# Optimization experiments

Measured on AMD Instinct MI355X. Metric: run time of the kernel, lower is better.

The kernel has to match this reference:

```python
import jax, jax.numpy as jnp
import numpy as np

D, K, H1, H2 = 768, 4, 512, 256
B = 16384

def layer_norm(x, g, b, eps=1e-5):
    mu = jnp.mean(x, axis=-1, keepdims=True)
    xc = x - mu
    var = jnp.mean(xc * xc, axis=-1, keepdims=True)
    return xc * jax.lax.rsqrt(var + eps) * g + b

def setup_inputs() -> dict:
    key = jax.random.key(0)
    ks = jax.random.split(key, 8)
    def lin(k, fan_in, fan_out):
        bound = 1.0 / np.sqrt(fan_in)
        kw, kb = jax.random.split(k)
        W = jax.random.uniform(kw, (fan_in, fan_out), jnp.float32, -bound, bound)
        b = jax.random.uniform(kb, (fan_out,), jnp.float32, -bound, bound)
        return W, b
    W1, b1 = lin(ks[0], D, H1)
    W2, b2 = lin(ks[1], H1, H2)
    Wd, bd = lin(ks[2], H2, K * D)
    Wa, ba = lin(ks[3], H2, D)
    return {
        "embeddings": jax.random.normal(ks[4], (B, D), jnp.float32),
        "W1": W1, "b1": b1, "g1": jnp.ones((H1,), jnp.float32), "be1": jnp.zeros((H1,), jnp.float32),
        "W2": W2, "b2": b2, "g2": jnp.ones((H2,), jnp.float32), "be2": jnp.zeros((H2,), jnp.float32),
        "Wd": Wd, "bd": bd, "Wa": Wa, "ba": ba,
    }

def _forward(embeddings, W1, b1, g1, be1, W2, b2, g2, be2, Wd, bd, Wa, ba):
    h = jax.nn.relu(layer_norm(embeddings @ W1 + b1, g1, be1))  # (B, H1)
    h = jax.nn.relu(layer_norm(h @ W2 + b2, g2, be2))           # (B, H2)
    W_flat = h @ Wd + bd                                         # (B, K*D)
    W = W_flat.reshape(-1, K, D)
    attn = jax.nn.softmax(h @ Wa + ba, axis=-1)                  # (B, D)
    W = W * attn[:, None, :]
    # sequential Gram-Schmidt over k (small fixed K, unrolled)
    ortho = []
    for i in range(K):
        v = W[:, i, :]
        for u in ortho:
            proj = jnp.sum(v * u, axis=-1, keepdims=True)
            v = v - proj * u
        norm = jnp.maximum(jnp.linalg.norm(v, axis=-1, keepdims=True), 1e-12)
        ortho.append(v / norm)
    W_ortho = jnp.stack(ortho, axis=1)  # (B, K, D)
    return W_ortho, attn

def reference(embeddings, W1, b1, g1, be1, W2, b2, g2, be2, Wd, bd, Wa, ba):
    return _forward(embeddings, W1, b1, g1, be1, W2, b2, g2, be2, Wd, bd, Wa, ba)
```

## Files before the change

kernel.cpp:

```cpp
#include <hip/hip_runtime.h>
#include <hip/hip_bf16.h>

#define BSZ 16384
#define DD  768
#define KK  4
#define NH1 512
#define NH2 256
#define ND  (KK * DD)

typedef __bf16 bf16x8 __attribute__((ext_vector_type(8)));
typedef float  f32x4  __attribute__((ext_vector_type(4)));

static __device__ __forceinline__ float bf2f(ushort u) {
    union { unsigned int i; float f; } v; v.i = (unsigned int)u << 16; return v.f;
}
static __device__ __forceinline__ ushort f2bf(float f) {
    return __bfloat16_as_ushort(__float2bfloat16(f));
}
static __device__ __forceinline__ void gload_lds16(const void* g, void* l) {
    __builtin_amdgcn_global_load_lds(
        (const __attribute__((address_space(1))) void*)g,
        (__attribute__((address_space(3))) void*)l, 16, 0, 0);
}

__global__ __launch_bounds__(256) void k_prep(
    const float* __restrict__ emb, ushort* __restrict__ embb,
    const float* __restrict__ W1, ushort* __restrict__ W1t,
    const float* __restrict__ W2, ushort* __restrict__ W2t,
    const float* __restrict__ Wd, ushort* __restrict__ Wdt,
    const float* __restrict__ Wa, ushort* __restrict__ Wat)
{
    __shared__ float tile[32][33];
    const int bid = blockIdx.x;
    const int t = threadIdx.x;

    if (bid < 2048) {
        const int n8 = BSZ * DD / 8;
        const int stride = 2048 * 256;
        for (int i = bid * 256 + t; i < n8; i += stride) {
            float4 a = *(const float4*)&emb[(size_t)i * 8];
            float4 b = *(const float4*)&emb[(size_t)i * 8 + 4];
            ushort u[8];
            u[0] = f2bf(a.x); u[1] = f2bf(a.y); u[2] = f2bf(a.z); u[3] = f2bf(a.w);
            u[4] = f2bf(b.x); u[5] = f2bf(b.y); u[6] = f2bf(b.z); u[7] = f2bf(b.w);
            *(int4*)&embb[(size_t)i * 8] = *(int4*)u;
        }
        return;
    }

    const float* src; ushort* dst; int R, C, rb0, cb0;
    if (bid < 2432)      { int l = bid - 2048; src = W1; dst = W1t; R = DD;  C = NH1;
                           cb0 = (l & 15) * 32; rb0 = (l >> 4) * 32; }
    else if (bid < 2560) { int l = bid - 2432; src = W2; dst = W2t; R = NH1; C = NH2;
                           cb0 = (l & 7) * 32;  rb0 = (l >> 3) * 32; }
    else if (bid < 3328) { int l = bid - 2560; src = Wd; dst = Wdt; R = NH2; C = ND;
                           cb0 = (l % 96) * 32; rb0 = (l / 96) * 32; }
    else                 { int l = bid - 3328; src = Wa; dst = Wat; R = NH2; C = DD;
                           cb0 = (l % 24) * 32; rb0 = (l / 24) * 32; }

    const int r = t >> 5, c = t & 31;
    #pragma unroll
    for (int i = 0; i < 4; ++i)
        tile[r + i * 8][c] = src[(size_t)(rb0 + r + i * 8) * C + cb0 + c];
    __syncthreads();
    #pragma unroll
    for (int i = 0; i < 4; ++i)
        dst[(size_t)(cb0 + r + i * 8) * R + rb0 + c] = f2bf(tile[c][r + i * 8]);
}

__global__ __launch_bounds__(256) void k1_gemm(
    const ushort* __restrict__ embb, const ushort* __restrict__ W1t,
    const float* __restrict__ b1, ushort* __restrict__ h1raw)
{
    __shared__ ushort smem[2 * 128 * 64];
    ushort* Asm = smem;
    ushort* Bsm = smem + 128 * 64;

    const int t    = threadIdx.x;
    const int lane = t & 63;
    const int wid  = t >> 6;
    const int wm   = wid >> 1;
    const int wn   = wid & 1;
    const int l16  = lane & 15;
    const int sl0  = lane >> 4;
    const int g4   = (lane >> 4) * 4;

    const int srow = lane >> 3;
    const int ssl  = (lane & 7) ^ srow;

    const int rb = blockIdx.y * 128;
    const int cb = blockIdx.x * 128;

    f32x4 acc[4][4] = {};

    for (int ks = 0; ks < 12; ++ks) {
        const int k0 = ks * 64;
        __syncthreads();
        #pragma unroll
        for (int i = 0; i < 4; ++i) {
            const int stripe = wid * 4 + i;
            const int row    = stripe * 8 + srow;
            gload_lds16(&embb[(size_t)(rb + row) * DD + k0 + ssl * 8],
                        &Asm[stripe * 512]);
            gload_lds16(&W1t [(size_t)(cb + row) * DD + k0 + ssl * 8],
                        &Bsm[stripe * 512]);
        }
        __syncthreads();

        #pragma unroll
        for (int kk = 0; kk < 2; ++kk) {
            const int slot = kk * 4 + sl0;
            bf16x8 af[4], bfr[4];
            #pragma unroll
            for (int m = 0; m < 4; ++m) {
                const int R = wm * 64 + m * 16 + l16;
                af[m] = *(const bf16x8*)&Asm[R * 64 + (slot ^ (R & 7)) * 8];
            }
            #pragma unroll
            for (int n = 0; n < 4; ++n) {
                const int R = wn * 64 + n * 16 + l16;
                bfr[n] = *(const bf16x8*)&Bsm[R * 64 + (slot ^ (R & 7)) * 8];
            }
            #pragma unroll
            for (int m = 0; m < 4; ++m)
                #pragma unroll
                for (int n = 0; n < 4; ++n)
                    acc[m][n] = __builtin_amdgcn_mfma_f32_16x16x32_bf16(
                        af[m], bfr[n], acc[m][n], 0, 0, 0);
        }
    }

    float bv[4];
    #pragma unroll
    for (int n = 0; n < 4; ++n)
        bv[n] = b1[cb + wn * 64 + n * 16 + l16];

    __syncthreads();
    #pragma unroll
    for (int m = 0; m < 4; ++m)
        #pragma unroll
        for (int n = 0; n < 4; ++n)
            #pragma unroll
            for (int j = 0; j < 4; ++j)
                smem[(wm * 64 + m * 16 + g4 + j) * 128 + wn * 64 + n * 16 + l16] =
                    f2bf(acc[m][n][j] + bv[n]);
    __syncthreads();
    #pragma unroll
    for (int i = 0; i < 8; ++i) {
        int ch  = t + i * 256;
        int row = ch >> 4;
        int q   = ch & 15;
        *(int4*)&h1raw[(size_t)(rb + row) * NH1 + cb + q * 8] =
            *(const int4*)&smem[row * 128 + q * 8];
    }
}

__global__ __launch_bounds__(512) void k2_mfma(
    const ushort* __restrict__ h1raw, const ushort* __restrict__ W2t,
    const float* __restrict__ g1, const float* __restrict__ be1,
    const float* __restrict__ b2, const float* __restrict__ g2,
    const float* __restrict__ be2, ushort* __restrict__ h2)
{
    __shared__ ushort Ah[8 * 2048];
    __shared__ ushort Bsm[256 * 64];
    __shared__ float red[8][32][2];
    __shared__ float stats[32][2];

    const int t    = threadIdx.x;
    const int lane = t & 63;
    const int wid  = t >> 6;
    const int l16  = lane & 15;
    const int sl0  = lane >> 4;
    const int g4   = (lane >> 4) * 4;
    const int rb   = blockIdx.x * 32;

    const int srow = lane >> 3;
    const int ssl  = (lane & 7) ^ srow;

    #pragma unroll
    for (int i = 0; i < 4; ++i) {
        const int s  = wid * 4 + i;
        const int ks = s >> 2;
        const int st = s & 3;
        const int row = st * 8 + srow;
        gload_lds16(&h1raw[(size_t)(rb + row) * NH1 + ks * 64 + ssl * 8],
                    &Ah[ks * 2048 + st * 512]);
    }
    __syncthreads();

    {
        const int r  = t >> 4;
        const int j  = t & 15;
        const int ks = j >> 1;
        const int hf = j & 1;
        ushort u[4][8];
        float s = 0.f, q2 = 0.f;
        #pragma unroll
        for (int qi = 0; qi < 4; ++qi) {
            const int q = hf * 4 + qi;
            *(int4*)u[qi] = *(const int4*)
                &Ah[ks * 2048 + (r >> 3) * 512 + (r & 7) * 64 + ((q ^ (r & 7)) * 8)];
            #pragma unroll
            for (int e = 0; e < 8; ++e) {
                float x = bf2f(u[qi][e]);
                s += x; q2 += x * x;
            }
        }
        #pragma unroll
        for (int off = 8; off; off >>= 1) {
            s  += __shfl_xor(s, off);
            q2 += __shfl_xor(q2, off);
        }
        const float mu  = s * (1.f / NH1);
        const float var = q2 * (1.f / NH1) - mu * mu;
        const float rs  = rsqrtf(var + 1e-5f);
        #pragma unroll
        for (int qi = 0; qi < 4; ++qi) {
            const int q = hf * 4 + qi;
            const int col = ks * 64 + q * 8;
            float gv[8], ev[8];
            *(float4*)&gv[0] = *(const float4*)&g1[col];
            *(float4*)&gv[4] = *(const float4*)&g1[col + 4];
            *(float4*)&ev[0] = *(const float4*)&be1[col];
            *(float4*)&ev[4] = *(const float4*)&be1[col + 4];
            #pragma unroll
            for (int e = 0; e < 8; ++e) {
                float x = bf2f(u[qi][e]);
                u[qi][e] = f2bf(fmaxf(fmaf((x - mu) * rs, gv[e], ev[e]), 0.f));
            }
            *(int4*)&Ah[ks * 2048 + (r >> 3) * 512 + (r & 7) * 64 + ((q ^ (r & 7)) * 8)]
                = *(int4*)u[qi];
        }
    }

    f32x4 acc[2][2] = {};

    for (int ks = 0; ks < 8; ++ks) {
        const int k0 = ks * 64;
        __syncthreads();
        #pragma unroll
        for (int i = 0; i < 4; ++i) {
            const int s   = wid * 4 + i;
            const int row = s * 8 + srow;
            gload_lds16(&W2t[(size_t)row * NH1 + k0 + ssl * 8],
                        &Bsm[s * 512]);
        }
        __syncthreads();

        #pragma unroll
        for (int kk = 0; kk < 2; ++kk) {
            const int slot = kk * 4 + sl0;
            bf16x8 af[2], bfr[2];
            #pragma unroll
            for (int m = 0; m < 2; ++m) {
                const int R = m * 16 + l16;
                af[m] = *(const bf16x8*)
                    &Ah[ks * 2048 + R * 64 + (slot ^ (R & 7)) * 8];
            }
            #pragma unroll
            for (int n = 0; n < 2; ++n) {
                const int R = wid * 32 + n * 16 + l16;
                bfr[n] = *(const bf16x8*)&Bsm[R * 64 + (slot ^ (R & 7)) * 8];
            }
            #pragma unroll
            for (int m = 0; m < 2; ++m)
                #pragma unroll
                for (int n = 0; n < 2; ++n)
                    acc[m][n] = __builtin_amdgcn_mfma_f32_16x16x32_bf16(
                        af[m], bfr[n], acc[m][n], 0, 0, 0);
        }
    }

    float bv[2];
    #pragma unroll
    for (int n = 0; n < 2; ++n) bv[n] = b2[wid * 32 + n * 16 + l16];
    #pragma unroll
    for (int m = 0; m < 2; ++m)
        #pragma unroll
        for (int n = 0; n < 2; ++n)
            #pragma unroll
            for (int j = 0; j < 4; ++j) acc[m][n][j] += bv[n];

    #pragma unroll
    for (int m = 0; m < 2; ++m)
        #pragma unroll
        for (int j = 0; j < 4; ++j) {
            float p = 0.f, q = 0.f;
            #pragma unroll
            for (int n = 0; n < 2; ++n) {
                float v = acc[m][n][j];
                p += v; q += v * v;
            }
            #pragma unroll
            for (int off = 8; off; off >>= 1) {
                p += __shfl_xor(p, off);
                q += __shfl_xor(q, off);
            }
            if (l16 == 0) {
                red[wid][m * 16 + g4 + j][0] = p;
                red[wid][m * 16 + g4 + j][1] = q;
            }
        }
    __syncthreads();
    if (t < 32) {
        float S = 0.f, S2 = 0.f;
        #pragma unroll
        for (int w = 0; w < 8; ++w) { S += red[w][t][0]; S2 += red[w][t][1]; }
        float mu  = S  * (1.f / NH2);
        float var = S2 * (1.f / NH2) - mu * mu;
        stats[t][0] = mu;
        stats[t][1] = rsqrtf(var + 1e-5f);
    }
    __syncthreads();

    float gv[2], ev[2];
    #pragma unroll
    for (int n = 0; n < 2; ++n) {
        int col = wid * 32 + n * 16 + l16;
        gv[n] = g2[col]; ev[n] = be2[col];
    }
    ushort* dst = h2 + (size_t)rb * NH2;
    #pragma unroll
    for (int m = 0; m < 2; ++m)
        #pragma unroll
        for (int j = 0; j < 4; ++j) {
            int row = m * 16 + g4 + j;
            float mu = stats[row][0], rs = stats[row][1];
            #pragma unroll
            for (int n = 0; n < 2; ++n) {
                float val = fmaxf(fmaf((acc[m][n][j] - mu) * rs, gv[n], ev[n]), 0.f);
                dst[(size_t)row * NH2 + wid * 32 + n * 16 + l16] = f2bf(val);
            }
        }
}

__global__ __launch_bounds__(256) void k_gemm_wd_mfma(
    const ushort* __restrict__ h2, const ushort* __restrict__ Wdt,
    const float* __restrict__ bd, ushort* __restrict__ outw)
{
    __shared__ ushort smem[2 * 128 * 64];
    ushort* Asm = smem;
    ushort* Bsm = smem + 128 * 64;

    const int t    = threadIdx.x;
    const int lane = t & 63;
    const int wid  = t >> 6;
    const int wm   = wid >> 1;
    const int wn   = wid & 1;
    const int l16  = lane & 15;
    const int sl0  = lane >> 4;
    const int g4   = (lane >> 4) * 4;

    const int srow = lane >> 3;
    const int ssl  = (lane & 7) ^ srow;

    const int rb = blockIdx.y * 128;
    const int cb = blockIdx.x * 128;

    f32x4 acc[4][4] = {};

    for (int ks = 0; ks < 4; ++ks) {
        const int k0 = ks * 64;
        __syncthreads();
        #pragma unroll
        for (int i = 0; i < 4; ++i) {
            const int stripe = wid * 4 + i;
            const int row    = stripe * 8 + srow;
            gload_lds16(&h2 [(size_t)(rb + row) * NH2 + k0 + ssl * 8],
                        &Asm[stripe * 512]);
            gload_lds16(&Wdt[(size_t)(cb + row) * NH2 + k0 + ssl * 8],
                        &Bsm[stripe * 512]);
        }
        __syncthreads();

        #pragma unroll
        for (int kk = 0; kk < 2; ++kk) {
            const int slot = kk * 4 + sl0;
            bf16x8 af[4], bfr[4];
            #pragma unroll
            for (int m = 0; m < 4; ++m) {
                const int R = wm * 64 + m * 16 + l16;
                af[m] = *(const bf16x8*)&Asm[R * 64 + (slot ^ (R & 7)) * 8];
            }
            #pragma unroll
            for (int n = 0; n < 4; ++n) {
                const int R = wn * 64 + n * 16 + l16;
                bfr[n] = *(const bf16x8*)&Bsm[R * 64 + (slot ^ (R & 7)) * 8];
            }
            #pragma unroll
            for (int m = 0; m < 4; ++m)
                #pragma unroll
                for (int n = 0; n < 4; ++n)
                    acc[m][n] = __builtin_amdgcn_mfma_f32_16x16x32_bf16(
                        af[m], bfr[n], acc[m][n], 0, 0, 0);
        }
    }

    float bv[4];
    #pragma unroll
    for (int n = 0; n < 4; ++n)
        bv[n] = bd[cb + wn * 64 + n * 16 + l16];

    __syncthreads();
    #pragma unroll
    for (int m = 0; m < 4; ++m)
        #pragma unroll
        for (int n = 0; n < 4; ++n)
            #pragma unroll
            for (int j = 0; j < 4; ++j)
                smem[(wm * 64 + m * 16 + g4 + j) * 128 + wn * 64 + n * 16 + l16] =
                    f2bf(acc[m][n][j] + bv[n]);
    __syncthreads();
    #pragma unroll
    for (int i = 0; i < 8; ++i) {
        int ch  = t + i * 256;
        int row = ch >> 4;
        int q   = ch & 15;
        *(int4*)&outw[(size_t)(rb + row) * 6144 + 3072 + cb + q * 8] =
            *(const int4*)&smem[row * 128 + q * 8];
    }
}

__global__ __launch_bounds__(512) void k_attn_gs_mfma(
    const ushort* __restrict__ h2, const ushort* __restrict__ Wat,
    const float* __restrict__ ba, float* __restrict__ out)
{
    __shared__ ushort Asm[64 * 64];
    __shared__ ushort Bsm[768 * 64];
    __shared__ float red[8][64];
    __shared__ float stats[64];

    const int t    = threadIdx.x;
    const int lane = t & 63;
    const int wid  = t >> 6;
    const int wm   = wid >> 2;
    const int wn   = wid & 3;
    const int l16  = lane & 15;
    const int sl0  = lane >> 4;
    const int g4   = (lane >> 4) * 4;
    const int rb   = blockIdx.x * 64;

    const int srow = lane >> 3;
    const int ssl  = (lane & 7) ^ srow;

    float* attn = out + (size_t)BSZ * (KK * DD);

    f32x4 acc[2][12] = {};

    for (int ks = 0; ks < 4; ++ks) {
        const int k0 = ks * 64;
        __syncthreads();
        {
            const int row = wid * 8 + srow;
            gload_lds16(&h2[(size_t)(rb + row) * NH2 + k0 + ssl * 8],
                        &Asm[wid * 512]);
        }
        #pragma unroll
        for (int i = 0; i < 12; ++i) {
            const int stripe = wid * 12 + i;
            const int row    = stripe * 8 + srow;
            gload_lds16(&Wat[(size_t)row * NH2 + k0 + ssl * 8],
                        &Bsm[stripe * 512]);
        }
        __syncthreads();

        #pragma unroll
        for (int kk = 0; kk < 2; ++kk) {
            const int slot = kk * 4 + sl0;
            bf16x8 af[2], bfr[12];
            #pragma unroll
            for (int m = 0; m < 2; ++m) {
                const int R = wm * 32 + m * 16 + l16;
                af[m] = *(const bf16x8*)&Asm[R * 64 + (slot ^ (R & 7)) * 8];
            }
            #pragma unroll
            for (int n = 0; n < 12; ++n) {
                const int R = wn * 192 + n * 16 + l16;
                bfr[n] = *(const bf16x8*)&Bsm[R * 64 + (slot ^ (R & 7)) * 8];
            }
            #pragma unroll
            for (int m = 0; m < 2; ++m)
                #pragma unroll
                for (int n = 0; n < 12; ++n)
                    acc[m][n] = __builtin_amdgcn_mfma_f32_16x16x32_bf16(
                        af[m], bfr[n], acc[m][n], 0, 0, 0);
        }
    }

    float bb[12];
    #pragma unroll
    for (int n = 0; n < 12; ++n) bb[n] = ba[wn * 192 + n * 16 + l16];
    #pragma unroll
    for (int m = 0; m < 2; ++m)
        #pragma unroll
        for (int n = 0; n < 12; ++n)
            #pragma unroll
            for (int j = 0; j < 4; ++j) acc[m][n][j] += bb[n];

    #pragma unroll
    for (int m = 0; m < 2; ++m)
        #pragma unroll
        for (int j = 0; j < 4; ++j) {
            float p = acc[m][0][j];
            #pragma unroll
            for (int n = 1; n < 12; ++n) p = fmaxf(p, acc[m][n][j]);
            #pragma unroll
            for (int off = 8; off; off >>= 1) p = fmaxf(p, __shfl_xor(p, off));
            if (l16 == 0) red[wid][wm * 32 + m * 16 + g4 + j] = p;
        }
    __syncthreads();
    if (t < 64) {
        const int w0 = (t >> 5) * 4;
        stats[t] = fmaxf(fmaxf(red[w0][t], red[w0 + 1][t]),
                         fmaxf(red[w0 + 2][t], red[w0 + 3][t]));
    }
    __syncthreads();
    #pragma unroll
    for (int m = 0; m < 2; ++m)
        #pragma unroll
        for (int j = 0; j < 4; ++j) {
            float M = stats[wm * 32 + m * 16 + g4 + j];
            float s = 0.f;
            #pragma unroll
            for (int n = 0; n < 12; ++n) {
                acc[m][n][j] = __expf(acc[m][n][j] - M);
                s += acc[m][n][j];
            }
            #pragma unroll
            for (int off = 8; off; off >>= 1) s += __shfl_xor(s, off);
            if (l16 == 0) red[wid][wm * 32 + m * 16 + g4 + j] = s;
        }
    __syncthreads();
    if (t < 64) {
        const int w0 = (t >> 5) * 4;
        stats[t] = 1.f / (red[w0][t] + red[w0 + 1][t] + red[w0 + 2][t] + red[w0 + 3][t]);
    }
    __syncthreads();

    float* stage = (float*)Bsm;
    #pragma unroll
    for (int h = 0; h < 2; ++h) {
        if (wm == h) {
            #pragma unroll
            for (int m = 0; m < 2; ++m)
                #pragma unroll
                for (int j = 0; j < 4; ++j) {
                    const int r = m * 16 + g4 + j;
                    const float inv = stats[h * 32 + r];
                    #pragma unroll
                    for (int n = 0; n < 12; ++n)
                        stage[r * 768 + wn * 192 + n * 16 + l16] = acc[m][n][j] * inv;
                }
        }
        __syncthreads();
        #pragma unroll
        for (int i = 0; i < 12; ++i) {
            int ch  = t + i * 512;
            int row = ch / 192;
            int q   = ch - row * 192;
            *(float4*)&attn[(size_t)(rb + h * 32 + row) * DD + q * 4] =
                *(const float4*)&stage[row * 768 + q * 4];
        }
        for (int rr = 0; rr < 4; ++rr) {
            const int rl = wid * 4 + rr;
            const size_t row = (size_t)rb + h * 32 + rl;
            float a[12];
            #pragma unroll
            for (int k = 0; k < 3; ++k)
                *(float4*)&a[k * 4] =
                    *(const float4*)&stage[rl * 768 + lane * 4 + 256 * k];

            const ushort* wsrc = (const ushort*)out + row * 6144 + 3072;
            float* Wf = out + row * (KK * DD);
            float w[4][12];
            #pragma unroll
            for (int i = 0; i < 4; ++i) {
                #pragma unroll
                for (int k = 0; k < 3; ++k) {
                    ushort4 uv = *(const ushort4*)&wsrc[i * DD + lane * 4 + 256 * k];
                    w[i][k * 4 + 0] = bf2f(uv.x) * a[k * 4 + 0];
                    w[i][k * 4 + 1] = bf2f(uv.y) * a[k * 4 + 1];
                    w[i][k * 4 + 2] = bf2f(uv.z) * a[k * 4 + 2];
                    w[i][k * 4 + 3] = bf2f(uv.w) * a[k * 4 + 3];
                }
            }
            #pragma unroll
            for (int i = 0; i < 4; ++i) {
                #pragma unroll
                for (int p = 0; p < i; ++p) {
                    float s2 = 0.f;
                    #pragma unroll
                    for (int j = 0; j < 12; ++j) s2 = fmaf(w[i][j], w[p][j], s2);
                    #pragma unroll
                    for (int off = 32; off; off >>= 1) s2 += __shfl_xor(s2, off);
                    #pragma unroll
                    for (int j = 0; j < 12; ++j) w[i][j] = fmaf(-s2, w[p][j], w[i][j]);
                }
                float n2 = 0.f;
                #pragma unroll
                for (int j = 0; j < 12; ++j) n2 = fmaf(w[i][j], w[i][j], n2);
                #pragma unroll
                for (int off = 32; off; off >>= 1) n2 += __shfl_xor(n2, off);
                float invn = 1.f / fmaxf(sqrtf(n2), 1e-12f);
                #pragma unroll
                for (int j = 0; j < 12; ++j) w[i][j] *= invn;
            }
            #pragma unroll
            for (int i = 0; i < 4; ++i) {
                #pragma unroll
                for (int k = 0; k < 3; ++k) {
                    float4 wv;
                    wv.x = w[i][k * 4 + 0]; wv.y = w[i][k * 4 + 1];
                    wv.z = w[i][k * 4 + 2]; wv.w = w[i][k * 4 + 3];
                    *(float4*)&Wf[i * DD + lane * 4 + 256 * k] = wv;
                }
            }
        }
        __syncthreads();
    }
}

extern "C" void kernel_launch(void* const* d_in, const int* in_sizes, int n_in,
                              void* d_out, int out_size, void* d_ws, size_t ws_size,
                              hipStream_t stream)
{
    const float* emb = (const float*)d_in[0];
    const float* W1  = (const float*)d_in[1];
    const float* b1  = (const float*)d_in[2];
    const float* g1  = (const float*)d_in[3];
    const float* be1 = (const float*)d_in[4];
    const float* W2  = (const float*)d_in[5];
    const float* b2  = (const float*)d_in[6];
    const float* g2  = (const float*)d_in[7];
    const float* be2 = (const float*)d_in[8];
    const float* Wd  = (const float*)d_in[9];
    const float* bd  = (const float*)d_in[10];
    const float* Wa  = (const float*)d_in[11];
    const float* ba  = (const float*)d_in[12];

    float* out = (float*)d_out;
    ushort* h1   = (ushort*)d_ws;
    ushort* h2   = h1 + (size_t)BSZ * NH1;
    ushort* Wdt  = h2 + (size_t)BSZ * NH2;
    ushort* W1t  = Wdt + (size_t)ND * NH2;
    ushort* W2t  = W1t + (size_t)NH1 * DD;
    ushort* Wat  = W2t + (size_t)NH2 * NH1;
    ushort* embb = Wat + (size_t)DD * NH2;

    hipLaunchKernelGGL(k_prep, dim3(3520), dim3(256), 0, stream,
                       emb, embb, W1, W1t, W2, W2t, Wd, Wdt, Wa, Wat);
    hipLaunchKernelGGL(k1_gemm, dim3(NH1 / 128, BSZ / 128), dim3(256), 0, stream,
                       embb, W1t, b1, h1);
    hipLaunchKernelGGL(k2_mfma, dim3(BSZ / 32), dim3(512), 0, stream,
                       h1, W2t, g1, be1, b2, g2, be2, h2);
    hipLaunchKernelGGL(k_gemm_wd_mfma, dim3(ND / 128, BSZ / 128), dim3(256), 0, stream,
                       h2, Wdt, bd, (ushort*)out);
    hipLaunchKernelGGL(k_attn_gs_mfma, dim3(BSZ / 64), dim3(512), 0, stream,
                       h2, Wat, ba, out);
}
```

Baseline: 174.2 us.

## Halve LDS footprint in attention-GS kernel by splitting N into two passes

The attention/Gram-Schmidt kernel now processes the 768 output columns in two 384-column halves, so the B tile in shared memory shrinks from 768x64 to 384x64 bf16. The staging epilogue is also reorganised into four 16-row passes instead of two 32-row passes, so it fits in the smaller buffer. The aim is to cut LDS use so more blocks can reside per CU and latency hiding improves. In exchange, h2 tiles are reloaded twice and the extra passes add more __syncthreads barriers.

```diff
diff --git a/kernel.cpp b/kernel.cpp
--- a/kernel.cpp
+++ b/kernel.cpp
@@ -426,7 +426,7 @@
     const float* __restrict__ ba, float* __restrict__ out)
 {
     __shared__ ushort Asm[64 * 64];
-    __shared__ ushort Bsm[768 * 64];
+    __shared__ ushort Bsm[384 * 64];
     __shared__ float red[8][64];
     __shared__ float stats[64];
 
@@ -447,49 +447,54 @@
 
     f32x4 acc[2][12] = {};
 
-    for (int ks = 0; ks < 4; ++ks) {
-        const int k0 = ks * 64;
-        __syncthreads();
-        {
-            const int row = wid * 8 + srow;
-            gload_lds16(&h2[(size_t)(rb + row) * NH2 + k0 + ssl * 8],
-                        &Asm[wid * 512]);
-        }
-        #pragma unroll
-        for (int i = 0; i < 12; ++i) {
-            const int stripe = wid * 12 + i;
-            const int row    = stripe * 8 + srow;
-            gload_lds16(&Wat[(size_t)row * NH2 + k0 + ssl * 8],
-                        &Bsm[stripe * 512]);
-        }
-        __syncthreads();
-
-        #pragma unroll
-        for (int kk = 0; kk < 2; ++kk) {
-            const int slot = kk * 4 + sl0;
-            bf16x8 af[2], bfr[12];
-            #pragma unroll
-            for (int m = 0; m < 2; ++m) {
-                const int R = wm * 32 + m * 16 + l16;
-                af[m] = *(const bf16x8*)&Asm[R * 64 + (slot ^ (R & 7)) * 8];
-            }
-            #pragma unroll
-            for (int n = 0; n < 12; ++n) {
-                const int R = wn * 192 + n * 16 + l16;
-                bfr[n] = *(const bf16x8*)&Bsm[R * 64 + (slot ^ (R & 7)) * 8];
-            }
-            #pragma unroll
-            for (int m = 0; m < 2; ++m)
-                #pragma unroll
-                for (int n = 0; n < 12; ++n)
-                    acc[m][n] = __builtin_amdgcn_mfma_f32_16x16x32_bf16(
-                        af[m], bfr[n], acc[m][n], 0, 0, 0);
+    for (int nh = 0; nh < 2; ++nh) {
+        for (int ks = 0; ks < 4; ++ks) {
+            const int k0 = ks * 64;
+            __syncthreads();
+            {
+                const int row = wid * 8 + srow;
+                gload_lds16(&h2[(size_t)(rb + row) * NH2 + k0 + ssl * 8],
+                            &Asm[wid * 512]);
+            }
+            #pragma unroll
+            for (int i = 0; i < 6; ++i) {
+                const int s   = wid * 6 + i;
+                const int row = nh * 384 + s * 8 + srow;
+                gload_lds16(&Wat[(size_t)row * NH2 + k0 + ssl * 8],
+                            &Bsm[s * 512]);
+            }
+            __syncthreads();
+
+            #pragma unroll
+            for (int kk = 0; kk < 2; ++kk) {
+                const int slot = kk * 4 + sl0;
+                bf16x8 af[2], bfr[6];
+                #pragma unroll
+                for (int m = 0; m < 2; ++m) {
+                    const int R = wm * 32 + m * 16 + l16;
+                    af[m] = *(const bf16x8*)&Asm[R * 64 + (slot ^ (R & 7)) * 8];
+                }
+                #pragma unroll
+                for (int n = 0; n < 6; ++n) {
+                    const int R = wn * 96 + n * 16 + l16;
+                    bfr[n] = *(const bf16x8*)&Bsm[R * 64 + (slot ^ (R & 7)) * 8];
+                }
+                #pragma unroll
+                for (int m = 0; m < 2; ++m)
+                    #pragma unroll
+                    for (int n = 0; n < 6; ++n)
+                        acc[m][nh * 6 + n] = __builtin_amdgcn_mfma_f32_16x16x32_bf16(
+                            af[m], bfr[n], acc[m][nh * 6 + n], 0, 0, 0);
+            }
         }
     }
 
     float bb[12];
     #pragma unroll
-    for (int n = 0; n < 12; ++n) bb[n] = ba[wn * 192 + n * 16 + l16];
+    for (int nh = 0; nh < 2; ++nh)
+        #pragma unroll
+        for (int n = 0; n < 6; ++n)
+            bb[nh * 6 + n] = ba[nh * 384 + wn * 96 + n * 16 + l16];
     #pragma unroll
     for (int m = 0; m < 2; ++m)
         #pragma unroll
@@ -539,31 +544,33 @@
 
     float* stage = (float*)Bsm;
     #pragma unroll
-    for (int h = 0; h < 2; ++h) {
-        if (wm == h) {
-            #pragma unroll
-            for (int m = 0; m < 2; ++m)
-                #pragma unroll
-                for (int j = 0; j < 4; ++j) {
-                    const int r = m * 16 + g4 + j;
-                    const float inv = stats[h * 32 + r];
+    for (int p = 0; p < 4; ++p) {
+        if (wm == (p >> 1)) {
+            const int m = p & 1;
+            #pragma unroll
+            for (int j = 0; j < 4; ++j) {
+                const int r = g4 + j;
+                const float inv = stats[p * 16 + r];
+                #pragma unroll
+                for (int nh = 0; nh < 2; ++nh)
                     #pragma unroll
-                    for (int n = 0; n < 12; ++n)
-                        stage[r * 768 + wn * 192 + n * 16 + l16] = acc[m][n][j] * inv;
-                }
-        }
-        __syncthreads();
-        #pragma unroll
-        for (int i = 0; i < 12; ++i) {
+                    for (int n = 0; n < 6; ++n)
+                        stage[r * 768 + nh * 384 + wn * 96 + n * 16 + l16] =
+                            acc[m][nh * 6 + n][j] * inv;
+            }
+        }
+        __syncthreads();
+        #pragma unroll
+        for (int i = 0; i < 6; ++i) {
             int ch  = t + i * 512;
             int row = ch / 192;
             int q   = ch - row * 192;
-            *(float4*)&attn[(size_t)(rb + h * 32 + row) * DD + q * 4] =
+            *(float4*)&attn[(size_t)(rb + p * 16 + row) * DD + q * 4] =
                 *(const float4*)&stage[row * 768 + q * 4];
         }
-        for (int rr = 0; rr < 4; ++rr) {
-            const int rl = wid * 4 + rr;
-            const size_t row = (size_t)rb + h * 32 + rl;
+        for (int rr = 0; rr < 2; ++rr) {
+            const int rl = wid * 2 + rr;
+            const size_t row = (size_t)rb + p * 16 + rl;
             float a[12];
             #pragma unroll
             for (int k = 0; k < 3; ++k)
@@ -587,14 +594,14 @@
             #pragma unroll
             for (int i = 0; i < 4; ++i) {
                 #pragma unroll
-                for (int p = 0; p < i; ++p) {
+                for (int pp = 0; pp < i; ++pp) {
                     float s2 = 0.f;
                     #pragma unroll
-                    for (int j = 0; j < 12; ++j) s2 = fmaf(w[i][j], w[p][j], s2);
+                    for (int j = 0; j < 12; ++j) s2 = fmaf(w[i][j], w[pp][j], s2);
                     #pragma unroll
                     for (int off = 32; off; off >>= 1) s2 += __shfl_xor(s2, off);
                     #pragma unroll
-                    for (int j = 0; j < 12; ++j) w[i][j] = fmaf(-s2, w[p][j], w[i][j]);
+                    for (int j = 0; j < 12; ++j) w[i][j] = fmaf(-s2, w[pp][j], w[i][j]);
                 }
                 float n2 = 0.f;
                 #pragma unroll
```

Measured after the change: 175.8 us. No clear change (+0.9%).
